# Kernel tuning notes

Hardware: AMD Instinct MI355X
Metric: run time of the kernel (lower is better)

## Reference

```python
import jax, jax.numpy as jnp
import numpy as np


def setup_inputs() -> dict:
    key = jax.random.key(0)
    k1, k2, k3 = jax.random.split(key, 3)
    N, C_in, H, W = 32, 64, 128, 128
    C_out, K = 128, 3
    fan_in = C_in * K * K
    bound = 1.0 / np.sqrt(fan_in)
    x = jax.random.normal(k1, (N, C_in, H, W), dtype=jnp.float32)
    weight = jax.random.uniform(k2, (C_out, C_in, K, K), dtype=jnp.float32, minval=-bound, maxval=bound)
    bias = jax.random.uniform(k3, (C_out,), dtype=jnp.float32, minval=-bound, maxval=bound)
    return {"x": x, "weight": weight, "bias": bias}


def reference(x, weight, bias):
    # conv2d, stride=1, padding=0 (VALID), NCHW / OIHW
    y = jax.lax.conv_general_dilated(
        x, weight,
        window_strides=(1, 1),
        padding='VALID',
        dimension_numbers=('NCHW', 'OIHW', 'NCHW'),
    )
    y = y + bias[None, :, None, None]          # [N, C_out, H_out, W_out]
    y = jnp.min(y, axis=1, keepdims=True)      # channel-wise min -> [N, 1, H_out, W_out]
    return jnp.tanh(jnp.tanh(y))
```

## Files before the change

### kernel.cpp

```cpp
#include <hip/hip_runtime.h>
#include <hip/hip_bf16.h>

typedef __attribute__((ext_vector_type(8))) short short8_t;
typedef __attribute__((ext_vector_type(4))) float floatx4;
typedef unsigned short ushort_t;
typedef unsigned int uint_t;

#define TILE_B 16896

#define RSTR 72
#define TSZ  (132 * RSTR)

__device__ __forceinline__ uint_t rne_u(float f) {
    uint_t u = __float_as_uint(f);
    return u + (0x7fffu + ((u >> 16) & 1u));
}
__device__ __forceinline__ uint_t pk2(float lo, float hi) {
    return __builtin_amdgcn_perm(rne_u(hi), rne_u(lo), 0x07060302u);
}

__global__ void w2_prepass(const float* __restrict__ w, ushort_t* __restrict__ w2) {
    int idx = blockIdx.x * 256 + threadIdx.x;
    int rd  = idx >> 12;
    int rem = idx & 4095;
    int co  = rem >> 5;
    int c32 = rem & 31;
    int khw = rd >> 1, half = rd & 1;
    int ci  = half * 32 + c32;
    w2[idx] = (ushort_t)(rne_u(w[co * 576 + ci * 9 + khw]) >> 16);
}

__global__ __launch_bounds__(256)
void x2_prepass(const float* __restrict__ x, ushort_t* __restrict__ x2) {
    __shared__ __align__(16) float lds[64 * 129];
    const int t = threadIdx.x;
    const int b = blockIdx.x;
    const int n = b >> 7, h = b & 127;
    const float* xp = x + ((size_t)n << 20) + (size_t)h * 128;
#pragma unroll
    for (int r = 0; r < 32; ++r) {
        int flat = r * 256 + t;
        int ci = flat >> 7, wq = flat & 127;
        lds[ci * 129 + wq] = xp[(size_t)ci * 16384 + wq];
    }
    __syncthreads();
    ushort_t* op = x2 + ((size_t)n * 128 + h) * 128 * 64;
#pragma unroll
    for (int r = 0; r < 4; ++r) {
        int id = r * 256 + t;
        int wq = id >> 3, q = id & 7;
        uint_t o[4];
#pragma unroll
        for (int qq = 0; qq < 4; ++qq)
            o[qq] = pk2(lds[(q * 8 + 2 * qq) * 129 + wq],
                        lds[(q * 8 + 2 * qq + 1) * 129 + wq]);
        *reinterpret_cast<uint4*>(op + (size_t)wq * 64 + q * 8) =
            make_uint4(o[0], o[1], o[2], o[3]);
    }
}

__global__ __launch_bounds__(512, 4)
void conv_v3(const ushort_t* __restrict__ x2, const ushort_t* __restrict__ w2,
             const float* __restrict__ bias, float* __restrict__ out)
{
    __shared__ __align__(16) ushort_t T[4 * (TILE_B / 2)];
    __shared__ __align__(16) float red[2][256];

    const int tid  = threadIdx.x;
    const int bid0 = blockIdx.x;
    const int bid  = (bid0 & 7) * 252 + (bid0 >> 3);
    const int n    = bid / 63;
    const int ho0  = (bid - n * 63) * 2;

    const int lane = tid & 63;
    const int wid  = tid >> 6;
    const int wm   = wid >> 1;
    const int wn   = wid & 1;
    const int r16  = lane & 15;
    const int quad = lane >> 4;

    const int voffB = ((lane >> 3) * 128) + (((lane & 7) ^ (lane >> 3)) * 16);
    const ushort_t* xrow = x2 + ((size_t)n * 128 + ho0) * 128 * 64;
#pragma unroll
    for (int s = 0; s < 4; ++s) {
#pragma unroll
        for (int k = 0; k < 2; ++k) {
            const int col0 = (wid * 2 + k) * 8;
            const char* g = (const char*)xrow + (size_t)s * 16384 + col0 * 128 + voffB;
            const ushort_t* l = &T[(s * TILE_B + col0 * 128) / 2];
            __builtin_amdgcn_global_load_lds(
                (const __attribute__((address_space(1))) uint_t*)g,
                (__attribute__((address_space(3))) uint_t*)l, 16, 0, 0);
        }
    }

    {
        const int s = tid >> 7, rem = tid & 127;
        reinterpret_cast<uint_t*>(T)[(s * TILE_B + (128 + (rem >> 5)) * 128) / 4 + (rem & 31)] = 0u;
    }

    floatx4 acc[4][4];
#pragma unroll
    for (int i = 0; i < 4; ++i)
#pragma unroll
        for (int j = 0; j < 4; ++j)
            acc[i][j] = (floatx4){0.f, 0.f, 0.f, 0.f};

    const ushort_t* w2base = w2 + (size_t)(wn * 64 + r16) * 32 + quad * 8;

    const int mc0 = (wm & 1) * 64 + r16;
    const int ms0 = wm >> 1;

    __syncthreads();

#pragma unroll
    for (int rd = 0; rd < 18; ++rd) {
        const int khw  = rd >> 1;
        const int kh   = khw / 3;
        const int kw   = khw - kh * 3;
        const int half = rd & 1;

        short8_t bfr[4];
        {
            const ushort_t* bb = w2base + rd * 4096;
#pragma unroll
            for (int t4 = 0; t4 < 4; ++t4)
                bfr[t4] = *reinterpret_cast<const short8_t*>(bb + t4 * 512);
        }

        short8_t afr[4];
        {
            const int c0 = mc0 + kw;
            const int abase = (ms0 + kh) * TILE_B + c0 * 128
                            + (((half * 4 + quad) ^ (c0 & 7)) * 16);
            const char* ap = (const char*)T + abase;
#pragma unroll
            for (int t4 = 0; t4 < 4; ++t4)
                afr[t4] = *reinterpret_cast<const short8_t*>(ap + t4 * 2048);
        }

#pragma unroll
        for (int tm = 0; tm < 4; ++tm)
#pragma unroll
            for (int tn = 0; tn < 4; ++tn)
                acc[tm][tn] = __builtin_amdgcn_mfma_f32_16x16x32_bf16(
                    afr[tm], bfr[tn], acc[tm][tn], 0, 0, 0);
    }

    float bvv[4];
#pragma unroll
    for (int tn = 0; tn < 4; ++tn)
        bvv[tn] = bias[wn * 64 + tn * 16 + r16];

#pragma unroll
    for (int tm = 0; tm < 4; ++tm) {
#pragma unroll
        for (int r = 0; r < 4; ++r) {
            float v = acc[tm][0][r] + bvv[0];
            v = fminf(v, acc[tm][1][r] + bvv[1]);
            v = fminf(v, acc[tm][2][r] + bvv[2]);
            v = fminf(v, acc[tm][3][r] + bvv[3]);
            v = fminf(v, __shfl_xor(v, 1, 64));
            v = fminf(v, __shfl_xor(v, 2, 64));
            v = fminf(v, __shfl_xor(v, 4, 64));
            v = fminf(v, __shfl_xor(v, 8, 64));
            if (r16 == 0)
                red[wn][wm * 64 + tm * 16 + quad * 4 + r] = v;
        }
    }
    __syncthreads();

    if (tid < 256) {
        const int r  = tid >> 7;
        const int wo = tid & 127;
        if (wo < 126) {
            float v = fminf(red[0][tid], red[1][tid]);
            v = tanhf(tanhf(v));
            out[((size_t)n * 126 + ho0 + r) * 126 + wo] = v;
        }
    }
}

template<bool USE_W2>
__global__ __launch_bounds__(512, 4)
void conv_min_tanh_kernel(const float* __restrict__ x,
                          const float* __restrict__ w,
                          const ushort_t* __restrict__ w2,
                          const float* __restrict__ bias,
                          float* __restrict__ out)
{
    __shared__ __align__(16) ushort_t T[4 * TSZ];
    __shared__ __align__(16) float red[2][256];

    const int tid  = threadIdx.x;
    const int bid0 = blockIdx.x;
    const int bid  = (bid0 & 7) * 252 + (bid0 >> 3);
    const int n    = bid / 63;
    const int ho0  = (bid - n * 63) * 2;

    const int tx = tid & 31;
    const int ty = tid >> 5;

    const int lane = tid & 63;
    const int wid  = tid >> 6;
    const int wm   = wid >> 1;
    const int wn   = wid & 1;
    const int r16  = lane & 15;
    const int quad = lane >> 4;

    const float* xbase = x + ((size_t)n << 20) + (size_t)ho0 * 128;

    auto load_row = [&](floatx4 (&dv)[4], const int s) {
#pragma unroll
        for (int j = 0; j < 4; ++j)
            dv[j] = *reinterpret_cast<const floatx4*>(
                xbase + (size_t)(ty * 4 + j) * 16384 + s * 128 + tx * 4);
    };
    auto conv_row = [&](floatx4 (&dv)[4], const int s) {
#pragma unroll
        for (int i = 0; i < 4; ++i) {
            uint2 u;
            u.x = pk2(dv[0][i], dv[1][i]);
            u.y = pk2(dv[2][i], dv[3][i]);
            const int c   = tx * 4 + i;
            const int swz = (ty >> 1) ^ ((c >> 3) & 7);
            *reinterpret_cast<uint2*>(&T[s * TSZ + c * RSTR + swz * 8 + (ty & 1) * 4]) = u;
        }
    };

    floatx4 dva[4], dvb[4];
    load_row(dva, 0);
    load_row(dvb, 1);

    for (int idx = tid; idx < 576; idx += 512) {
        int s = idx / 144, o = idx - s * 144;
        reinterpret_cast<uint_t*>(T)[s * (TSZ / 2) + (128 * RSTR) / 2 + o] = 0u;
    }

    conv_row(dva, 0);
    load_row(dva, 2);
    conv_row(dvb, 1);
    load_row(dvb, 3);
    conv_row(dva, 2);
    conv_row(dvb, 3);

    floatx4 acc[4][4];
#pragma unroll
    for (int i = 0; i < 4; ++i)
#pragma unroll
        for (int j = 0; j < 4; ++j)
            acc[i][j] = (floatx4){0.f, 0.f, 0.f, 0.f};

    const ushort_t* w2base = w2 + (size_t)(wn * 64 + r16) * 32 + quad * 8;
    const float*    wbase  = w + (size_t)(wn * 64 + r16) * 576;

    __syncthreads();

#pragma unroll
    for (int rd = 0; rd < 18; ++rd) {
        const int khw  = rd >> 1;
        const int kh   = khw / 3;
        const int kw   = khw - kh * 3;
        const int half = rd & 1;

        short8_t bfr[4];
        if (USE_W2) {
            const ushort_t* bb = w2base + rd * 4096;
#pragma unroll
            for (int t4 = 0; t4 < 4; ++t4)
                bfr[t4] = *reinterpret_cast<const short8_t*>(bb + t4 * 512);
        } else {
#pragma unroll
            for (int t4 = 0; t4 < 4; ++t4) {
                const float* wp = wbase + (size_t)t4 * (16 * 576)
                                + (size_t)(half * 32 + quad * 8) * 9 + khw;
                short8_t b;
#pragma unroll
                for (int q = 0; q < 4; ++q) {
                    uint_t u = pk2(wp[(2 * q) * 9], wp[(2 * q + 1) * 9]);
                    b[2 * q]     = (short)(u & 0xffffu);
                    b[2 * q + 1] = (short)(u >> 16);
                }
                bfr[t4] = b;
            }
        }

        short8_t afr[4];
#pragma unroll
        for (int t4 = 0; t4 < 4; ++t4) {
            const int m  = wm * 64 + t4 * 16 + r16;
            const int s  = (m >> 7) + kh;
            const int c  = (m & 127) + kw;
            const int sw = (half * 4 + quad) ^ ((c >> 3) & 7);
            afr[t4] = *reinterpret_cast<const short8_t*>(&T[s * TSZ + c * RSTR + sw * 8]);
        }
#pragma unroll
        for (int tm = 0; tm < 4; ++tm)
#pragma unroll
            for (int tn = 0; tn < 4; ++tn)
                acc[tm][tn] = __builtin_amdgcn_mfma_f32_16x16x32_bf16(
                    afr[tm], bfr[tn], acc[tm][tn], 0, 0, 0);
    }

    float bvv[4];
#pragma unroll
    for (int tn = 0; tn < 4; ++tn)
        bvv[tn] = bias[wn * 64 + tn * 16 + r16];

#pragma unroll
    for (int tm = 0; tm < 4; ++tm) {
#pragma unroll
        for (int r = 0; r < 4; ++r) {
            float v = acc[tm][0][r] + bvv[0];
            v = fminf(v, acc[tm][1][r] + bvv[1]);
            v = fminf(v, acc[tm][2][r] + bvv[2]);
            v = fminf(v, acc[tm][3][r] + bvv[3]);
            v = fminf(v, __shfl_xor(v, 1, 64));
            v = fminf(v, __shfl_xor(v, 2, 64));
            v = fminf(v, __shfl_xor(v, 4, 64));
            v = fminf(v, __shfl_xor(v, 8, 64));
            if (r16 == 0)
                red[wn][wm * 64 + tm * 16 + quad * 4 + r] = v;
        }
    }
    __syncthreads();

    if (tid < 256) {
        const int r  = tid >> 7;
        const int wo = tid & 127;
        if (wo < 126) {
            float v = fminf(red[0][tid], red[1][tid]);
            v = tanhf(tanhf(v));
            out[((size_t)n * 126 + ho0 + r) * 126 + wo] = v;
        }
    }
}

extern "C" void kernel_launch(void* const* d_in, const int* in_sizes, int n_in,
                              void* d_out, int out_size, void* d_ws, size_t ws_size,
                              hipStream_t stream) {
    const float* x    = (const float*)d_in[0];
    const float* w    = (const float*)d_in[1];
    const float* bias = (const float*)d_in[2];
    float* out = (float*)d_out;

    const size_t X2B = (size_t)32 * 128 * 128 * 64 * 2;
    const size_t W2B = (size_t)73728 * 2;

    if (ws_size >= X2B + W2B) {
        ushort_t* x2 = (ushort_t*)d_ws;
        ushort_t* w2 = (ushort_t*)((char*)d_ws + X2B);
        x2_prepass<<<dim3(4096), dim3(256), 0, stream>>>(x, x2);
        w2_prepass<<<dim3(288), dim3(256), 0, stream>>>(w, w2);
        conv_v3<<<dim3(2016), dim3(512), 0, stream>>>(x2, w2, bias, out);
    } else if (ws_size >= W2B) {
        ushort_t* w2 = (ushort_t*)d_ws;
        w2_prepass<<<dim3(288), dim3(256), 0, stream>>>(w, w2);
        conv_min_tanh_kernel<true><<<dim3(2016), dim3(512), 0, stream>>>(x, w, (ushort_t*)d_ws, bias, out);
    } else {
        conv_min_tanh_kernel<false><<<dim3(2016), dim3(512), 0, stream>>>(x, w, nullptr, bias, out);
    }
}
```

Baseline: 284.5 us.

## Process six output rows per block with rolling LDS ring and fused prepass

Each conv block now computes three consecutive output row-pairs, keeping a 4-slot ring of bf16 input rows in LDS. It refills the next two rows via global_load_lds partway through each pass, so each input row is loaded about once instead of roughly twice. Weight fragments are software-prefetched one step ahead, and the x and w bf16 prepasses are merged into one launch. The grid shrinks from 2016 to 672 blocks, which reduces parallelism and tail balance, and the mid-loop barrier may stall waves.

```diff
diff --git a/kernel.cpp b/kernel.cpp
--- a/kernel.cpp
+++ b/kernel.cpp
@@ -17,6 +17,208 @@
 }
 __device__ __forceinline__ uint_t pk2(float lo, float hi) {
     return __builtin_amdgcn_perm(rne_u(hi), rne_u(lo), 0x07060302u);
+}
+
+__global__ __launch_bounds__(256)
+void prepass_fused(const float* __restrict__ x, const float* __restrict__ w,
+                   ushort_t* __restrict__ x2, ushort_t* __restrict__ w2)
+{
+    __shared__ __align__(16) float lds[64 * 129];
+    const int t = threadIdx.x;
+    const int b = blockIdx.x;
+    if (b >= 4096) {
+        int idx = (b - 4096) * 256 + t;
+        int rd  = idx >> 12;
+        int rem = idx & 4095;
+        int co  = rem >> 5;
+        int c32 = rem & 31;
+        int khw = rd >> 1, half = rd & 1;
+        int ci  = half * 32 + c32;
+        w2[idx] = (ushort_t)(rne_u(w[co * 576 + ci * 9 + khw]) >> 16);
+        return;
+    }
+    const int n = b >> 7, h = b & 127;
+    const float* xp = x + ((size_t)n << 20) + (size_t)h * 128;
+#pragma unroll
+    for (int r = 0; r < 16; ++r) {
+        int flat = r * 256 + t;
+        int ci = flat >> 6, wh = flat & 63;
+        float2 v = *reinterpret_cast<const float2*>(xp + (size_t)ci * 16384 + wh * 2);
+        lds[ci * 129 + wh * 2]     = v.x;
+        lds[ci * 129 + wh * 2 + 1] = v.y;
+    }
+    __syncthreads();
+    ushort_t* op = x2 + ((size_t)n * 128 + h) * 8192;
+#pragma unroll
+    for (int r = 0; r < 4; ++r) {
+        int id = r * 256 + t;
+        int wq = id >> 3, q = id & 7;
+        uint_t o[4];
+#pragma unroll
+        for (int qq = 0; qq < 4; ++qq)
+            o[qq] = pk2(lds[(q * 8 + 2 * qq) * 129 + wq],
+                        lds[(q * 8 + 2 * qq + 1) * 129 + wq]);
+        *reinterpret_cast<uint4*>(op + (size_t)wq * 64 + q * 8) =
+            make_uint4(o[0], o[1], o[2], o[3]);
+    }
+}
+
+__global__ __launch_bounds__(512, 4)
+void conv_v4(const ushort_t* __restrict__ x2, const ushort_t* __restrict__ w2,
+             const float* __restrict__ bias, float* __restrict__ out)
+{
+    __shared__ __align__(16) ushort_t T[4 * (TILE_B / 2)];
+    __shared__ __align__(16) float red[2][256];
+
+    const int tid  = threadIdx.x;
+    const int bid0 = blockIdx.x;
+    const int bid  = (bid0 & 7) * 84 + (bid0 >> 3);
+    const int n    = bid / 21;
+    const int pg   = bid - n * 21;
+    const int ho0  = pg * 6;
+
+    const int lane = tid & 63;
+    const int wid  = tid >> 6;
+    const int wm   = wid >> 1;
+    const int wn   = wid & 1;
+    const int r16  = lane & 15;
+    const int quad = lane >> 4;
+    const int ms0  = wm >> 1;
+    const int mc0  = (wm & 1) * 64 + r16;
+
+    const int voffB = ((lane >> 3) * 128) + (((lane & 7) ^ (lane >> 3)) * 16);
+    const ushort_t* xrow = x2 + ((size_t)n * 128 + ho0) * 8192;
+
+#pragma unroll
+    for (int s = 0; s < 4; ++s)
+#pragma unroll
+        for (int k = 0; k < 2; ++k) {
+            const int col0 = (wid * 2 + k) * 8;
+            const char* g = (const char*)xrow + (size_t)s * 16384 + col0 * 128 + voffB;
+            const ushort_t* l = &T[(s * TILE_B + col0 * 128) / 2];
+            __builtin_amdgcn_global_load_lds(
+                (const __attribute__((address_space(1))) uint_t*)g,
+                (__attribute__((address_space(3))) uint_t*)l, 16, 0, 0);
+        }
+
+    {
+        const int s = tid >> 7, rem = tid & 127;
+        reinterpret_cast<uint_t*>(T)[(s * TILE_B + (128 + (rem >> 5)) * 128) / 4 + (rem & 31)] = 0u;
+    }
+
+    floatx4 acc[4][4];
+#pragma unroll
+    for (int i = 0; i < 4; ++i)
+#pragma unroll
+        for (int j = 0; j < 4; ++j)
+            acc[i][j] = (floatx4){0.f, 0.f, 0.f, 0.f};
+
+    const ushort_t* w2base = w2 + (size_t)(wn * 64 + r16) * 32 + quad * 8;
+
+    short8_t bcur[4], bnxt[4];
+#pragma unroll
+    for (int t4 = 0; t4 < 4; ++t4)
+        bcur[t4] = *reinterpret_cast<const short8_t*>(w2base + t4 * 512);
+
+    __syncthreads();
+
+#pragma unroll 1
+    for (int j = 0; j < 3; ++j) {
+#pragma unroll
+        for (int rd = 0; rd < 18; ++rd) {
+            {
+                const int nxt = (rd + 1) % 18;
+                const ushort_t* bb = w2base + nxt * 4096;
+#pragma unroll
+                for (int t4 = 0; t4 < 4; ++t4)
+                    bnxt[t4] = *reinterpret_cast<const short8_t*>(bb + t4 * 512);
+            }
+            const int khw  = rd >> 1;
+            const int kh   = khw / 3;
+            const int kw   = khw - kh * 3;
+            const int half = rd & 1;
+
+            short8_t afr[4];
+            {
+                const int sl = (2 * j + kh + ms0) & 3;
+                const int c0 = mc0 + kw;
+                const int abase = sl * TILE_B + c0 * 128
+                                + (((half * 4 + quad) ^ (c0 & 7)) * 16);
+                const char* ap = (const char*)T + abase;
+#pragma unroll
+                for (int t4 = 0; t4 < 4; ++t4)
+                    afr[t4] = *reinterpret_cast<const short8_t*>(ap + t4 * 2048);
+            }
+#pragma unroll
+            for (int tm = 0; tm < 4; ++tm)
+#pragma unroll
+                for (int tn = 0; tn < 4; ++tn)
+                    acc[tm][tn] = __builtin_amdgcn_mfma_f32_16x16x32_bf16(
+                        afr[tm], bcur[tn], acc[tm][tn], 0, 0, 0);
+#pragma unroll
+            for (int t4 = 0; t4 < 4; ++t4)
+                bcur[t4] = bnxt[t4];
+
+            if (rd == 11) {
+                __syncthreads();
+                if (j < 2) {
+                    const int lr = 2 * j + 4;
+#pragma unroll
+                    for (int rr = 0; rr < 2; ++rr)
+#pragma unroll
+                        for (int k = 0; k < 2; ++k) {
+                            const int col0 = (wid * 2 + k) * 8;
+                            const char* g = (const char*)xrow
+                                + (size_t)(lr + rr) * 16384 + col0 * 128 + voffB;
+                            const ushort_t* l =
+                                &T[(((lr + rr) & 3) * TILE_B + col0 * 128) / 2];
+                            __builtin_amdgcn_global_load_lds(
+                                (const __attribute__((address_space(1))) uint_t*)g,
+                                (__attribute__((address_space(3))) uint_t*)l, 16, 0, 0);
+                        }
+                }
+            }
+        }
+
+        float bvv[4];
+#pragma unroll
+        for (int tn = 0; tn < 4; ++tn)
+            bvv[tn] = bias[wn * 64 + tn * 16 + r16];
+
+#pragma unroll
+        for (int tm = 0; tm < 4; ++tm) {
+#pragma unroll
+            for (int r = 0; r < 4; ++r) {
+                float v = acc[tm][0][r] + bvv[0];
+                v = fminf(v, acc[tm][1][r] + bvv[1]);
+                v = fminf(v, acc[tm][2][r] + bvv[2]);
+                v = fminf(v, acc[tm][3][r] + bvv[3]);
+                v = fminf(v, __shfl_xor(v, 1, 64));
+                v = fminf(v, __shfl_xor(v, 2, 64));
+                v = fminf(v, __shfl_xor(v, 4, 64));
+                v = fminf(v, __shfl_xor(v, 8, 64));
+                if (r16 == 0)
+                    red[wn][wm * 64 + tm * 16 + quad * 4 + r] = v;
+            }
+        }
+        __syncthreads();
+
+        if (tid < 256) {
+            const int r  = tid >> 7;
+            const int wo = tid & 127;
+            if (wo < 126) {
+                float v = fminf(red[0][tid], red[1][tid]);
+                v = tanhf(tanhf(v));
+                out[((size_t)n * 126 + ho0 + 2 * j + r) * 126 + wo] = v;
+            }
+        }
+
+#pragma unroll
+        for (int i = 0; i < 4; ++i)
+#pragma unroll
+            for (int k = 0; k < 4; ++k)
+                acc[i][k] = (floatx4){0.f, 0.f, 0.f, 0.f};
+    }
 }
 
 __global__ void w2_prepass(const float* __restrict__ w, ushort_t* __restrict__ w2) {
@@ -30,40 +232,15 @@
     w2[idx] = (ushort_t)(rne_u(w[co * 576 + ci * 9 + khw]) >> 16);
 }
 
-__global__ __launch_bounds__(256)
-void x2_prepass(const float* __restrict__ x, ushort_t* __restrict__ x2) {
-    __shared__ __align__(16) float lds[64 * 129];
-    const int t = threadIdx.x;
-    const int b = blockIdx.x;
-    const int n = b >> 7, h = b & 127;
-    const float* xp = x + ((size_t)n << 20) + (size_t)h * 128;
-#pragma unroll
-    for (int r = 0; r < 32; ++r) {
-        int flat = r * 256 + t;
-        int ci = flat >> 7, wq = flat & 127;
-        lds[ci * 129 + wq] = xp[(size_t)ci * 16384 + wq];
-    }
-    __syncthreads();
-    ushort_t* op = x2 + ((size_t)n * 128 + h) * 128 * 64;
-#pragma unroll
-    for (int r = 0; r < 4; ++r) {
-        int id = r * 256 + t;
-        int wq = id >> 3, q = id & 7;
-        uint_t o[4];
-#pragma unroll
-        for (int qq = 0; qq < 4; ++qq)
-            o[qq] = pk2(lds[(q * 8 + 2 * qq) * 129 + wq],
-                        lds[(q * 8 + 2 * qq + 1) * 129 + wq]);
-        *reinterpret_cast<uint4*>(op + (size_t)wq * 64 + q * 8) =
-            make_uint4(o[0], o[1], o[2], o[3]);
-    }
-}
-
+template<bool USE_W2>
 __global__ __launch_bounds__(512, 4)
-void conv_v3(const ushort_t* __restrict__ x2, const ushort_t* __restrict__ w2,
-             const float* __restrict__ bias, float* __restrict__ out)
+void conv_min_tanh_kernel(const float* __restrict__ x,
+                          const float* __restrict__ w,
+                          const ushort_t* __restrict__ w2,
+                          const float* __restrict__ bias,
+                          float* __restrict__ out)
 {
-    __shared__ __align__(16) ushort_t T[4 * (TILE_B / 2)];
+    __shared__ __align__(16) ushort_t T[4 * TSZ];
     __shared__ __align__(16) float red[2][256];
 
     const int tid  = threadIdx.x;
@@ -71,6 +248,9 @@
     const int bid  = (bid0 & 7) * 252 + (bid0 >> 3);
     const int n    = bid / 63;
     const int ho0  = (bid - n * 63) * 2;
+
+    const int tx = tid & 31;
+    const int ty = tid >> 5;
 
     const int lane = tid & 63;
     const int wid  = tid >> 6;
@@ -79,25 +259,41 @@
     const int r16  = lane & 15;
     const int quad = lane >> 4;
 
-    const int voffB = ((lane >> 3) * 128) + (((lane & 7) ^ (lane >> 3)) * 16);
-    const ushort_t* xrow = x2 + ((size_t)n * 128 + ho0) * 128 * 64;
-#pragma unroll
-    for (int s = 0; s < 4; ++s) {
-#pragma unroll
-        for (int k = 0; k < 2; ++k) {
-            const int col0 = (wid * 2 + k) * 8;
-            const char* g = (const char*)xrow + (size_t)s * 16384 + col0 * 128 + voffB;
-            const ushort_t* l = &T[(s * TILE_B + col0 * 128) / 2];
-            __builtin_amdgcn_global_load_lds(
-                (const __attribute__((address_space(1))) uint_t*)g,
-                (__attribute__((address_space(3))) uint_t*)l, 16, 0, 0);
-        }
-    }
-
-    {
-        const int s = tid >> 7, rem = tid & 127;
-        reinterpret_cast<uint_t*>(T)[(s * TILE_B + (128 + (rem >> 5)) * 128) / 4 + (rem & 31)] = 0u;
-    }
+    const float* xbase = x + ((size_t)n << 20) + (size_t)ho0 * 128;
+
+    auto load_row = [&](floatx4 (&dv)[4], const int s) {
+#pragma unroll
+        for (int j = 0; j < 4; ++j)
+            dv[j] = *reinterpret_cast<const floatx4*>(
+                xbase + (size_t)(ty * 4 + j) * 16384 + s * 128 + tx * 4);
+    };
+    auto conv_row = [&](floatx4 (&dv)[4], const int s) {
+#pragma unroll
+        for (int i = 0; i < 4; ++i) {
+            uint2 u;
+            u.x = pk2(dv[0][i], dv[1][i]);
+            u.y = pk2(dv[2][i], dv[3][i]);
+            const int c   = tx * 4 + i;
+            const int swz = (ty >> 1) ^ ((c >> 3) & 7);
+            *reinterpret_cast<uint2*>(&T[s * TSZ + c * RSTR + swz * 8 + (ty & 1) * 4]) = u;
+        }
+    };
+
+    floatx4 dva[4], dvb[4];
+    load_row(dva, 0);
+    load_row(dvb, 1);
+
+    for (int idx = tid; idx < 576; idx += 512) {
+        int s = idx / 144, o = idx - s * 144;
+        reinterpret_cast<uint_t*>(T)[s * (TSZ / 2) + (128 * RSTR) / 2 + o] = 0u;
+    }
+
+    conv_row(dva, 0);
+    load_row(dva, 2);
+    conv_row(dvb, 1);
+    load_row(dvb, 3);
+    conv_row(dva, 2);
+    conv_row(dvb, 3);
 
     floatx4 acc[4][4];
 #pragma unroll
@@ -107,9 +303,7 @@
             acc[i][j] = (floatx4){0.f, 0.f, 0.f, 0.f};
 
     const ushort_t* w2base = w2 + (size_t)(wn * 64 + r16) * 32 + quad * 8;
-
-    const int mc0 = (wm & 1) * 64 + r16;
-    const int ms0 = wm >> 1;
+    const float*    wbase  = w + (size_t)(wn * 64 + r16) * 576;
 
     __syncthreads();
 
@@ -121,24 +315,36 @@
         const int half = rd & 1;
 
         short8_t bfr[4];
-        {
+        if (USE_W2) {
             const ushort_t* bb = w2base + rd * 4096;
 #pragma unroll
             for (int t4 = 0; t4 < 4; ++t4)
                 bfr[t4] = *reinterpret_cast<const short8_t*>(bb + t4 * 512);
+        } else {
+#pragma unroll
+            for (int t4 = 0; t4 < 4; ++t4) {
+                const float* wp = wbase + (size_t)t4 * (16 * 576)
+                                + (size_t)(half * 32 + quad * 8) * 9 + khw;
+                short8_t b;
+#pragma unroll
+                for (int q = 0; q < 4; ++q) {
+                    uint_t u = pk2(wp[(2 * q) * 9], wp[(2 * q + 1) * 9]);
+                    b[2 * q]     = (short)(u & 0xffffu);
+                    b[2 * q + 1] = (short)(u >> 16);
+                }
+                bfr[t4] = b;
+            }
         }
 
         short8_t afr[4];
-        {
-            const int c0 = mc0 + kw;
-            const int abase = (ms0 + kh) * TILE_B + c0 * 128
-                            + (((half * 4 + quad) ^ (c0 & 7)) * 16);
-            const char* ap = (const char*)T + abase;
-#pragma unroll
-            for (int t4 = 0; t4 < 4; ++t4)
-                afr[t4] = *reinterpret_cast<const short8_t*>(ap + t4 * 2048);
-        }
-
+#pragma unroll
+        for (int t4 = 0; t4 < 4; ++t4) {
+            const int m  = wm * 64 + t4 * 16 + r16;
+            const int s  = (m >> 7) + kh;
+            const int c  = (m & 127) + kw;
+            const int sw = (half * 4 + quad) ^ ((c >> 3) & 7);
+            afr[t4] = *reinterpret_cast<const short8_t*>(&T[s * TSZ + c * RSTR + sw * 8]);
+        }
 #pragma unroll
         for (int tm = 0; tm < 4; ++tm)
 #pragma unroll
@@ -181,161 +387,6 @@
     }
 }
 
-template<bool USE_W2>
-__global__ __launch_bounds__(512, 4)
-void conv_min_tanh_kernel(const float* __restrict__ x,
-                          const float* __restrict__ w,
-                          const ushort_t* __restrict__ w2,
-                          const float* __restrict__ bias,
-                          float* __restrict__ out)
-{
-    __shared__ __align__(16) ushort_t T[4 * TSZ];
-    __shared__ __align__(16) float red[2][256];
-
-    const int tid  = threadIdx.x;
-    const int bid0 = blockIdx.x;
-    const int bid  = (bid0 & 7) * 252 + (bid0 >> 3);
-    const int n    = bid / 63;
-    const int ho0  = (bid - n * 63) * 2;
-
-    const int tx = tid & 31;
-    const int ty = tid >> 5;
-
-    const int lane = tid & 63;
-    const int wid  = tid >> 6;
-    const int wm   = wid >> 1;
-    const int wn   = wid & 1;
-    const int r16  = lane & 15;
-    const int quad = lane >> 4;
-
-    const float* xbase = x + ((size_t)n << 20) + (size_t)ho0 * 128;
-
-    auto load_row = [&](floatx4 (&dv)[4], const int s) {
-#pragma unroll
-        for (int j = 0; j < 4; ++j)
-            dv[j] = *reinterpret_cast<const floatx4*>(
-                xbase + (size_t)(ty * 4 + j) * 16384 + s * 128 + tx * 4);
-    };
-    auto conv_row = [&](floatx4 (&dv)[4], const int s) {
-#pragma unroll
-        for (int i = 0; i < 4; ++i) {
-            uint2 u;
-            u.x = pk2(dv[0][i], dv[1][i]);
-            u.y = pk2(dv[2][i], dv[3][i]);
-            const int c   = tx * 4 + i;
-            const int swz = (ty >> 1) ^ ((c >> 3) & 7);
-            *reinterpret_cast<uint2*>(&T[s * TSZ + c * RSTR + swz * 8 + (ty & 1) * 4]) = u;
-        }
-    };
-
-    floatx4 dva[4], dvb[4];
-    load_row(dva, 0);
-    load_row(dvb, 1);
-
-    for (int idx = tid; idx < 576; idx += 512) {
-        int s = idx / 144, o = idx - s * 144;
-        reinterpret_cast<uint_t*>(T)[s * (TSZ / 2) + (128 * RSTR) / 2 + o] = 0u;
-    }
-
-    conv_row(dva, 0);
-    load_row(dva, 2);
-    conv_row(dvb, 1);
-    load_row(dvb, 3);
-    conv_row(dva, 2);
-    conv_row(dvb, 3);
-
-    floatx4 acc[4][4];
-#pragma unroll
-    for (int i = 0; i < 4; ++i)
-#pragma unroll
-        for (int j = 0; j < 4; ++j)
-            acc[i][j] = (floatx4){0.f, 0.f, 0.f, 0.f};
-
-    const ushort_t* w2base = w2 + (size_t)(wn * 64 + r16) * 32 + quad * 8;
-    const float*    wbase  = w + (size_t)(wn * 64 + r16) * 576;
-
-    __syncthreads();
-
-#pragma unroll
-    for (int rd = 0; rd < 18; ++rd) {
-        const int khw  = rd >> 1;
-        const int kh   = khw / 3;
-        const int kw   = khw - kh * 3;
-        const int half = rd & 1;
-
-        short8_t bfr[4];
-        if (USE_W2) {
-            const ushort_t* bb = w2base + rd * 4096;
-#pragma unroll
-            for (int t4 = 0; t4 < 4; ++t4)
-                bfr[t4] = *reinterpret_cast<const short8_t*>(bb + t4 * 512);
-        } else {
-#pragma unroll
-            for (int t4 = 0; t4 < 4; ++t4) {
-                const float* wp = wbase + (size_t)t4 * (16 * 576)
-                                + (size_t)(half * 32 + quad * 8) * 9 + khw;
-                short8_t b;
-#pragma unroll
-                for (int q = 0; q < 4; ++q) {
-                    uint_t u = pk2(wp[(2 * q) * 9], wp[(2 * q + 1) * 9]);
-                    b[2 * q]     = (short)(u & 0xffffu);
-                    b[2 * q + 1] = (short)(u >> 16);
-                }
-                bfr[t4] = b;
-            }
-        }
-
-        short8_t afr[4];
-#pragma unroll
-        for (int t4 = 0; t4 < 4; ++t4) {
-            const int m  = wm * 64 + t4 * 16 + r16;
-            const int s  = (m >> 7) + kh;
-            const int c  = (m & 127) + kw;
-            const int sw = (half * 4 + quad) ^ ((c >> 3) & 7);
-            afr[t4] = *reinterpret_cast<const short8_t*>(&T[s * TSZ + c * RSTR + sw * 8]);
-        }
-#pragma unroll
-        for (int tm = 0; tm < 4; ++tm)
-#pragma unroll
-            for (int tn = 0; tn < 4; ++tn)
-                acc[tm][tn] = __builtin_amdgcn_mfma_f32_16x16x32_bf16(
-                    afr[tm], bfr[tn], acc[tm][tn], 0, 0, 0);
-    }
-
-    float bvv[4];
-#pragma unroll
-    for (int tn = 0; tn < 4; ++tn)
-        bvv[tn] = bias[wn * 64 + tn * 16 + r16];
-
-#pragma unroll
-    for (int tm = 0; tm < 4; ++tm) {
-#pragma unroll
-        for (int r = 0; r < 4; ++r) {
-            float v = acc[tm][0][r] + bvv[0];
-            v = fminf(v, acc[tm][1][r] + bvv[1]);
-            v = fminf(v, acc[tm][2][r] + bvv[2]);
-            v = fminf(v, acc[tm][3][r] + bvv[3]);
-            v = fminf(v, __shfl_xor(v, 1, 64));
-            v = fminf(v, __shfl_xor(v, 2, 64));
-            v = fminf(v, __shfl_xor(v, 4, 64));
-            v = fminf(v, __shfl_xor(v, 8, 64));
-            if (r16 == 0)
-                red[wn][wm * 64 + tm * 16 + quad * 4 + r] = v;
-        }
-    }
-    __syncthreads();
-
-    if (tid < 256) {
-        const int r  = tid >> 7;
-        const int wo = tid & 127;
-        if (wo < 126) {
-            float v = fminf(red[0][tid], red[1][tid]);
-            v = tanhf(tanhf(v));
-            out[((size_t)n * 126 + ho0 + r) * 126 + wo] = v;
-        }
-    }
-}
-
 extern "C" void kernel_launch(void* const* d_in, const int* in_sizes, int n_in,
                               void* d_out, int out_size, void* d_ws, size_t ws_size,
                               hipStream_t stream) {
@@ -350,13 +401,12 @@
     if (ws_size >= X2B + W2B) {
         ushort_t* x2 = (ushort_t*)d_ws;
         ushort_t* w2 = (ushort_t*)((char*)d_ws + X2B);
-        x2_prepass<<<dim3(4096), dim3(256), 0, stream>>>(x, x2);
-        w2_prepass<<<dim3(288), dim3(256), 0, stream>>>(w, w2);
-        conv_v3<<<dim3(2016), dim3(512), 0, stream>>>(x2, w2, bias, out);
+        prepass_fused<<<dim3(4096 + 288), dim3(256), 0, stream>>>(x, w, x2, w2);
+        conv_v4<<<dim3(672), dim3(512), 0, stream>>>(x2, w2, bias, out);
     } else if (ws_size >= W2B) {
         ushort_t* w2 = (ushort_t*)d_ws;
         w2_prepass<<<dim3(288), dim3(256), 0, stream>>>(w, w2);
-        conv_min_tanh_kernel<true><<<dim3(2016), dim3(512), 0, stream>>>(x, w, (ushort_t*)d_ws, bias, out);
+        conv_min_tanh_kernel<true><<<dim3(2016), dim3(512), 0, stream>>>(x, w, w2, bias, out);
     } else {
         conv_min_tanh_kernel<false><<<dim3(2016), dim3(512), 0, stream>>>(x, w, nullptr, bias, out);
     }
```

After: 555.6 us. 1.95x slower.

## Fuse input/weight prepasses and shrink conv tile to one output row per block

Applied to the files above, without the earlier changes.

The x and weight bf16 conversion prepasses are merged into a single launch, with float2 loads in the x transpose, removing one kernel launch. The conv kernel now computes one output row per block instead of two. It loads 3 input rows into LDS instead of 4, halving the accumulator registers and LDS per block and raising the occupancy hint from 4 to 6 blocks. This trades more input-row reloads across blocks (3 rows per output row instead of 2) for higher occupancy, twice as many blocks and less register pressure.

```diff
diff --git a/kernel.cpp b/kernel.cpp
--- a/kernel.cpp
+++ b/kernel.cpp
@@ -17,6 +17,166 @@
 }
 __device__ __forceinline__ uint_t pk2(float lo, float hi) {
     return __builtin_amdgcn_perm(rne_u(hi), rne_u(lo), 0x07060302u);
+}
+
+__global__ __launch_bounds__(256)
+void prepass_fused(const float* __restrict__ x, const float* __restrict__ w,
+                   ushort_t* __restrict__ x2, ushort_t* __restrict__ w2)
+{
+    __shared__ __align__(16) float lds[64 * 129];
+    const int t = threadIdx.x;
+    const int b = blockIdx.x;
+    if (b >= 4096) {
+        int idx = (b - 4096) * 256 + t;
+        int rd  = idx >> 12;
+        int rem = idx & 4095;
+        int co  = rem >> 5;
+        int c32 = rem & 31;
+        int khw = rd >> 1, half = rd & 1;
+        int ci  = half * 32 + c32;
+        w2[idx] = (ushort_t)(rne_u(w[co * 576 + ci * 9 + khw]) >> 16);
+        return;
+    }
+    const int n = b >> 7, h = b & 127;
+    const float* xp = x + ((size_t)n << 20) + (size_t)h * 128;
+#pragma unroll
+    for (int r = 0; r < 16; ++r) {
+        int flat = r * 256 + t;
+        int ci = flat >> 6, wh = flat & 63;
+        float2 v = *reinterpret_cast<const float2*>(xp + (size_t)ci * 16384 + wh * 2);
+        lds[ci * 129 + wh * 2]     = v.x;
+        lds[ci * 129 + wh * 2 + 1] = v.y;
+    }
+    __syncthreads();
+    ushort_t* op = x2 + ((size_t)n * 128 + h) * 8192;
+#pragma unroll
+    for (int r = 0; r < 4; ++r) {
+        int id = r * 256 + t;
+        int wq = id >> 3, q = id & 7;
+        uint_t o[4];
+#pragma unroll
+        for (int qq = 0; qq < 4; ++qq)
+            o[qq] = pk2(lds[(q * 8 + 2 * qq) * 129 + wq],
+                        lds[(q * 8 + 2 * qq + 1) * 129 + wq]);
+        *reinterpret_cast<uint4*>(op + (size_t)wq * 64 + q * 8) =
+            make_uint4(o[0], o[1], o[2], o[3]);
+    }
+}
+
+__global__ __launch_bounds__(512, 6)
+void conv_v5(const ushort_t* __restrict__ x2, const ushort_t* __restrict__ w2,
+             const float* __restrict__ bias, float* __restrict__ out)
+{
+    __shared__ __align__(16) ushort_t T[3 * (TILE_B / 2)];
+    __shared__ __align__(16) float red[2][128];
+
+    const int tid  = threadIdx.x;
+    const int bid0 = blockIdx.x;
+    const int bid  = (bid0 & 7) * 504 + (bid0 >> 3);
+    const int n    = bid / 126;
+    const int ho   = bid - n * 126;
+
+    const int lane = tid & 63;
+    const int wid  = tid >> 6;
+    const int wm   = wid >> 1;
+    const int wn   = wid & 1;
+    const int r16  = lane & 15;
+    const int quad = lane >> 4;
+    const int mc0  = wm * 32 + r16;
+
+    const int voffB = ((lane >> 3) * 128) + (((lane & 7) ^ (lane >> 3)) * 16);
+    const ushort_t* xrow = x2 + ((size_t)n * 128 + ho) * 8192;
+
+#pragma unroll
+    for (int s = 0; s < 3; ++s)
+#pragma unroll
+        for (int k = 0; k < 2; ++k) {
+            const int col0 = (wid * 2 + k) * 8;
+            const char* g = (const char*)xrow + (size_t)s * 16384 + col0 * 128 + voffB;
+            const ushort_t* l = &T[(s * TILE_B + col0 * 128) / 2];
+            __builtin_amdgcn_global_load_lds(
+                (const __attribute__((address_space(1))) uint_t*)g,
+                (__attribute__((address_space(3))) uint_t*)l, 16, 0, 0);
+        }
+
+    if (tid < 384) {
+        const int s = tid / 128, rem = tid & 127;
+        reinterpret_cast<uint_t*>(T)[(s * TILE_B + (128 + (rem >> 5)) * 128) / 4 + (rem & 31)] = 0u;
+    }
+
+    floatx4 acc[2][4];
+#pragma unroll
+    for (int i = 0; i < 2; ++i)
+#pragma unroll
+        for (int j = 0; j < 4; ++j)
+            acc[i][j] = (floatx4){0.f, 0.f, 0.f, 0.f};
+
+    const ushort_t* w2base = w2 + (size_t)(wn * 64 + r16) * 32 + quad * 8;
+
+    __syncthreads();
+
+#pragma unroll
+    for (int rd = 0; rd < 18; ++rd) {
+        const int khw  = rd >> 1;
+        const int kh   = khw / 3;
+        const int kw   = khw - kh * 3;
+        const int half = rd & 1;
+
+        short8_t bfr[4];
+        {
+            const ushort_t* bb = w2base + rd * 4096;
+#pragma unroll
+            for (int t4 = 0; t4 < 4; ++t4)
+                bfr[t4] = *reinterpret_cast<const short8_t*>(bb + t4 * 512);
+        }
+
+        short8_t afr[2];
+        {
+            const int c0 = mc0 + kw;
+            const int abase = kh * TILE_B + c0 * 128
+                            + (((half * 4 + quad) ^ (c0 & 7)) * 16);
+            const char* ap = (const char*)T + abase;
+#pragma unroll
+            for (int t4 = 0; t4 < 2; ++t4)
+                afr[t4] = *reinterpret_cast<const short8_t*>(ap + t4 * 2048);
+        }
+
+#pragma unroll
+        for (int tm = 0; tm < 2; ++tm)
+#pragma unroll
+            for (int tn = 0; tn < 4; ++tn)
+                acc[tm][tn] = __builtin_amdgcn_mfma_f32_16x16x32_bf16(
+                    afr[tm], bfr[tn], acc[tm][tn], 0, 0, 0);
+    }
+
+    float bvv[4];
+#pragma unroll
+    for (int tn = 0; tn < 4; ++tn)
+        bvv[tn] = bias[wn * 64 + tn * 16 + r16];
+
+#pragma unroll
+    for (int tm = 0; tm < 2; ++tm) {
+#pragma unroll
+        for (int r = 0; r < 4; ++r) {
+            float v = acc[tm][0][r] + bvv[0];
+            v = fminf(v, acc[tm][1][r] + bvv[1]);
+            v = fminf(v, acc[tm][2][r] + bvv[2]);
+            v = fminf(v, acc[tm][3][r] + bvv[3]);
+            v = fminf(v, __shfl_xor(v, 1, 64));
+            v = fminf(v, __shfl_xor(v, 2, 64));
+            v = fminf(v, __shfl_xor(v, 4, 64));
+            v = fminf(v, __shfl_xor(v, 8, 64));
+            if (r16 == 0)
+                red[wn][wm * 32 + tm * 16 + quad * 4 + r] = v;
+        }
+    }
+    __syncthreads();
+
+    if (tid < 126) {
+        float v = fminf(red[0][tid], red[1][tid]);
+        v = tanhf(tanhf(v));
+        out[((size_t)n * 126 + ho) * 126 + tid] = v;
+    }
 }
 
 __global__ void w2_prepass(const float* __restrict__ w, ushort_t* __restrict__ w2) {
@@ -30,40 +190,15 @@
     w2[idx] = (ushort_t)(rne_u(w[co * 576 + ci * 9 + khw]) >> 16);
 }
 
-__global__ __launch_bounds__(256)
-void x2_prepass(const float* __restrict__ x, ushort_t* __restrict__ x2) {
-    __shared__ __align__(16) float lds[64 * 129];
-    const int t = threadIdx.x;
-    const int b = blockIdx.x;
-    const int n = b >> 7, h = b & 127;
-    const float* xp = x + ((size_t)n << 20) + (size_t)h * 128;
-#pragma unroll
-    for (int r = 0; r < 32; ++r) {
-        int flat = r * 256 + t;
-        int ci = flat >> 7, wq = flat & 127;
-        lds[ci * 129 + wq] = xp[(size_t)ci * 16384 + wq];
-    }
-    __syncthreads();
-    ushort_t* op = x2 + ((size_t)n * 128 + h) * 128 * 64;
-#pragma unroll
-    for (int r = 0; r < 4; ++r) {
-        int id = r * 256 + t;
-        int wq = id >> 3, q = id & 7;
-        uint_t o[4];
-#pragma unroll
-        for (int qq = 0; qq < 4; ++qq)
-            o[qq] = pk2(lds[(q * 8 + 2 * qq) * 129 + wq],
-                        lds[(q * 8 + 2 * qq + 1) * 129 + wq]);
-        *reinterpret_cast<uint4*>(op + (size_t)wq * 64 + q * 8) =
-            make_uint4(o[0], o[1], o[2], o[3]);
-    }
-}
-
+template<bool USE_W2>
 __global__ __launch_bounds__(512, 4)
-void conv_v3(const ushort_t* __restrict__ x2, const ushort_t* __restrict__ w2,
-             const float* __restrict__ bias, float* __restrict__ out)
+void conv_min_tanh_kernel(const float* __restrict__ x,
+                          const float* __restrict__ w,
+                          const ushort_t* __restrict__ w2,
+                          const float* __restrict__ bias,
+                          float* __restrict__ out)
 {
-    __shared__ __align__(16) ushort_t T[4 * (TILE_B / 2)];
+    __shared__ __align__(16) ushort_t T[4 * TSZ];
     __shared__ __align__(16) float red[2][256];
 
     const int tid  = threadIdx.x;
@@ -71,6 +206,9 @@
     const int bid  = (bid0 & 7) * 252 + (bid0 >> 3);
     const int n    = bid / 63;
     const int ho0  = (bid - n * 63) * 2;
+
+    const int tx = tid & 31;
+    const int ty = tid >> 5;
 
     const int lane = tid & 63;
     const int wid  = tid >> 6;
@@ -79,25 +217,41 @@
     const int r16  = lane & 15;
     const int quad = lane >> 4;
 
-    const int voffB = ((lane >> 3) * 128) + (((lane & 7) ^ (lane >> 3)) * 16);
-    const ushort_t* xrow = x2 + ((size_t)n * 128 + ho0) * 128 * 64;
-#pragma unroll
-    for (int s = 0; s < 4; ++s) {
-#pragma unroll
-        for (int k = 0; k < 2; ++k) {
-            const int col0 = (wid * 2 + k) * 8;
-            const char* g = (const char*)xrow + (size_t)s * 16384 + col0 * 128 + voffB;
-            const ushort_t* l = &T[(s * TILE_B + col0 * 128) / 2];
-            __builtin_amdgcn_global_load_lds(
-                (const __attribute__((address_space(1))) uint_t*)g,
-                (__attribute__((address_space(3))) uint_t*)l, 16, 0, 0);
-        }
-    }
-
-    {
-        const int s = tid >> 7, rem = tid & 127;
-        reinterpret_cast<uint_t*>(T)[(s * TILE_B + (128 + (rem >> 5)) * 128) / 4 + (rem & 31)] = 0u;
-    }
+    const float* xbase = x + ((size_t)n << 20) + (size_t)ho0 * 128;
+
+    auto load_row = [&](floatx4 (&dv)[4], const int s) {
+#pragma unroll
+        for (int j = 0; j < 4; ++j)
+            dv[j] = *reinterpret_cast<const floatx4*>(
+                xbase + (size_t)(ty * 4 + j) * 16384 + s * 128 + tx * 4);
+    };
+    auto conv_row = [&](floatx4 (&dv)[4], const int s) {
+#pragma unroll
+        for (int i = 0; i < 4; ++i) {
+            uint2 u;
+            u.x = pk2(dv[0][i], dv[1][i]);
+            u.y = pk2(dv[2][i], dv[3][i]);
+            const int c   = tx * 4 + i;
+            const int swz = (ty >> 1) ^ ((c >> 3) & 7);
+            *reinterpret_cast<uint2*>(&T[s * TSZ + c * RSTR + swz * 8 + (ty & 1) * 4]) = u;
+        }
+    };
+
+    floatx4 dva[4], dvb[4];
+    load_row(dva, 0);
+    load_row(dvb, 1);
+
+    for (int idx = tid; idx < 576; idx += 512) {
+        int s = idx / 144, o = idx - s * 144;
+        reinterpret_cast<uint_t*>(T)[s * (TSZ / 2) + (128 * RSTR) / 2 + o] = 0u;
+    }
+
+    conv_row(dva, 0);
+    load_row(dva, 2);
+    conv_row(dvb, 1);
+    load_row(dvb, 3);
+    conv_row(dva, 2);
+    conv_row(dvb, 3);
 
     floatx4 acc[4][4];
 #pragma unroll
@@ -107,9 +261,7 @@
             acc[i][j] = (floatx4){0.f, 0.f, 0.f, 0.f};
 
     const ushort_t* w2base = w2 + (size_t)(wn * 64 + r16) * 32 + quad * 8;
-
-    const int mc0 = (wm & 1) * 64 + r16;
-    const int ms0 = wm >> 1;
+    const float*    wbase  = w + (size_t)(wn * 64 + r16) * 576;
 
     __syncthreads();
 
@@ -121,24 +273,36 @@
         const int half = rd & 1;
 
         short8_t bfr[4];
-        {
+        if (USE_W2) {
             const ushort_t* bb = w2base + rd * 4096;
 #pragma unroll
             for (int t4 = 0; t4 < 4; ++t4)
                 bfr[t4] = *reinterpret_cast<const short8_t*>(bb + t4 * 512);
+        } else {
+#pragma unroll
+            for (int t4 = 0; t4 < 4; ++t4) {
+                const float* wp = wbase + (size_t)t4 * (16 * 576)
+                                + (size_t)(half * 32 + quad * 8) * 9 + khw;
+                short8_t b;
+#pragma unroll
+                for (int q = 0; q < 4; ++q) {
+                    uint_t u = pk2(wp[(2 * q) * 9], wp[(2 * q + 1) * 9]);
+                    b[2 * q]     = (short)(u & 0xffffu);
+                    b[2 * q + 1] = (short)(u >> 16);
+                }
+                bfr[t4] = b;
+            }
         }
 
         short8_t afr[4];
-        {
-            const int c0 = mc0 + kw;
-            const int abase = (ms0 + kh) * TILE_B + c0 * 128
-                            + (((half * 4 + quad) ^ (c0 & 7)) * 16);
-            const char* ap = (const char*)T + abase;
-#pragma unroll
-            for (int t4 = 0; t4 < 4; ++t4)
-                afr[t4] = *reinterpret_cast<const short8_t*>(ap + t4 * 2048);
-        }
-
+#pragma unroll
+        for (int t4 = 0; t4 < 4; ++t4) {
+            const int m  = wm * 64 + t4 * 16 + r16;
+            const int s  = (m >> 7) + kh;
+            const int c  = (m & 127) + kw;
+            const int sw = (half * 4 + quad) ^ ((c >> 3) & 7);
+            afr[t4] = *reinterpret_cast<const short8_t*>(&T[s * TSZ + c * RSTR + sw * 8]);
+        }
 #pragma unroll
         for (int tm = 0; tm < 4; ++tm)
 #pragma unroll
@@ -181,161 +345,6 @@
     }
 }
 
-template<bool USE_W2>
-__global__ __launch_bounds__(512, 4)
-void conv_min_tanh_kernel(const float* __restrict__ x,
-                          const float* __restrict__ w,
-                          const ushort_t* __restrict__ w2,
-                          const float* __restrict__ bias,
-                          float* __restrict__ out)
-{
-    __shared__ __align__(16) ushort_t T[4 * TSZ];
-    __shared__ __align__(16) float red[2][256];
-
-    const int tid  = threadIdx.x;
-    const int bid0 = blockIdx.x;
-    const int bid  = (bid0 & 7) * 252 + (bid0 >> 3);
-    const int n    = bid / 63;
-    const int ho0  = (bid - n * 63) * 2;
-
-    const int tx = tid & 31;
-    const int ty = tid >> 5;
-
-    const int lane = tid & 63;
-    const int wid  = tid >> 6;
-    const int wm   = wid >> 1;
-    const int wn   = wid & 1;
-    const int r16  = lane & 15;
-    const int quad = lane >> 4;
-
-    const float* xbase = x + ((size_t)n << 20) + (size_t)ho0 * 128;
-
-    auto load_row = [&](floatx4 (&dv)[4], const int s) {
-#pragma unroll
-        for (int j = 0; j < 4; ++j)
-            dv[j] = *reinterpret_cast<const floatx4*>(
-                xbase + (size_t)(ty * 4 + j) * 16384 + s * 128 + tx * 4);
-    };
-    auto conv_row = [&](floatx4 (&dv)[4], const int s) {
-#pragma unroll
-        for (int i = 0; i < 4; ++i) {
-            uint2 u;
-            u.x = pk2(dv[0][i], dv[1][i]);
-            u.y = pk2(dv[2][i], dv[3][i]);
-            const int c   = tx * 4 + i;
-            const int swz = (ty >> 1) ^ ((c >> 3) & 7);
-            *reinterpret_cast<uint2*>(&T[s * TSZ + c * RSTR + swz * 8 + (ty & 1) * 4]) = u;
-        }
-    };
-
-    floatx4 dva[4], dvb[4];
-    load_row(dva, 0);
-    load_row(dvb, 1);
-
-    for (int idx = tid; idx < 576; idx += 512) {
-        int s = idx / 144, o = idx - s * 144;
-        reinterpret_cast<uint_t*>(T)[s * (TSZ / 2) + (128 * RSTR) / 2 + o] = 0u;
-    }
-
-    conv_row(dva, 0);
-    load_row(dva, 2);
-    conv_row(dvb, 1);
-    load_row(dvb, 3);
-    conv_row(dva, 2);
-    conv_row(dvb, 3);
-
-    floatx4 acc[4][4];
-#pragma unroll
-    for (int i = 0; i < 4; ++i)
-#pragma unroll
-        for (int j = 0; j < 4; ++j)
-            acc[i][j] = (floatx4){0.f, 0.f, 0.f, 0.f};
-
-    const ushort_t* w2base = w2 + (size_t)(wn * 64 + r16) * 32 + quad * 8;
-    const float*    wbase  = w + (size_t)(wn * 64 + r16) * 576;
-
-    __syncthreads();
-
-#pragma unroll
-    for (int rd = 0; rd < 18; ++rd) {
-        const int khw  = rd >> 1;
-        const int kh   = khw / 3;
-        const int kw   = khw - kh * 3;
-        const int half = rd & 1;
-
-        short8_t bfr[4];
-        if (USE_W2) {
-            const ushort_t* bb = w2base + rd * 4096;
-#pragma unroll
-            for (int t4 = 0; t4 < 4; ++t4)
-                bfr[t4] = *reinterpret_cast<const short8_t*>(bb + t4 * 512);
-        } else {
-#pragma unroll
-            for (int t4 = 0; t4 < 4; ++t4) {
-                const float* wp = wbase + (size_t)t4 * (16 * 576)
-                                + (size_t)(half * 32 + quad * 8) * 9 + khw;
-                short8_t b;
-#pragma unroll
-                for (int q = 0; q < 4; ++q) {
-                    uint_t u = pk2(wp[(2 * q) * 9], wp[(2 * q + 1) * 9]);
-                    b[2 * q]     = (short)(u & 0xffffu);
-                    b[2 * q + 1] = (short)(u >> 16);
-                }
-                bfr[t4] = b;
-            }
-        }
-
-        short8_t afr[4];
-#pragma unroll
-        for (int t4 = 0; t4 < 4; ++t4) {
-            const int m  = wm * 64 + t4 * 16 + r16;
-            const int s  = (m >> 7) + kh;
-            const int c  = (m & 127) + kw;
-            const int sw = (half * 4 + quad) ^ ((c >> 3) & 7);
-            afr[t4] = *reinterpret_cast<const short8_t*>(&T[s * TSZ + c * RSTR + sw * 8]);
-        }
-#pragma unroll
-        for (int tm = 0; tm < 4; ++tm)
-#pragma unroll
-            for (int tn = 0; tn < 4; ++tn)
-                acc[tm][tn] = __builtin_amdgcn_mfma_f32_16x16x32_bf16(
-                    afr[tm], bfr[tn], acc[tm][tn], 0, 0, 0);
-    }
-
-    float bvv[4];
-#pragma unroll
-    for (int tn = 0; tn < 4; ++tn)
-        bvv[tn] = bias[wn * 64 + tn * 16 + r16];
-
-#pragma unroll
-    for (int tm = 0; tm < 4; ++tm) {
-#pragma unroll
-        for (int r = 0; r < 4; ++r) {
-            float v = acc[tm][0][r] + bvv[0];
-            v = fminf(v, acc[tm][1][r] + bvv[1]);
-            v = fminf(v, acc[tm][2][r] + bvv[2]);
-            v = fminf(v, acc[tm][3][r] + bvv[3]);
-            v = fminf(v, __shfl_xor(v, 1, 64));
-            v = fminf(v, __shfl_xor(v, 2, 64));
-            v = fminf(v, __shfl_xor(v, 4, 64));
-            v = fminf(v, __shfl_xor(v, 8, 64));
-            if (r16 == 0)
-                red[wn][wm * 64 + tm * 16 + quad * 4 + r] = v;
-        }
-    }
-    __syncthreads();
-
-    if (tid < 256) {
-        const int r  = tid >> 7;
-        const int wo = tid & 127;
-        if (wo < 126) {
-            float v = fminf(red[0][tid], red[1][tid]);
-            v = tanhf(tanhf(v));
-            out[((size_t)n * 126 + ho0 + r) * 126 + wo] = v;
-        }
-    }
-}
-
 extern "C" void kernel_launch(void* const* d_in, const int* in_sizes, int n_in,
                               void* d_out, int out_size, void* d_ws, size_t ws_size,
                               hipStream_t stream) {
@@ -350,13 +359,12 @@
     if (ws_size >= X2B + W2B) {
         ushort_t* x2 = (ushort_t*)d_ws;
         ushort_t* w2 = (ushort_t*)((char*)d_ws + X2B);
-        x2_prepass<<<dim3(4096), dim3(256), 0, stream>>>(x, x2);
-        w2_prepass<<<dim3(288), dim3(256), 0, stream>>>(w, w2);
-        conv_v3<<<dim3(2016), dim3(512), 0, stream>>>(x2, w2, bias, out);
+        prepass_fused<<<dim3(4096 + 288), dim3(256), 0, stream>>>(x, w, x2, w2);
+        conv_v5<<<dim3(4032), dim3(512), 0, stream>>>(x2, w2, bias, out);
     } else if (ws_size >= W2B) {
         ushort_t* w2 = (ushort_t*)d_ws;
         w2_prepass<<<dim3(288), dim3(256), 0, stream>>>(w, w2);
-        conv_min_tanh_kernel<true><<<dim3(2016), dim3(512), 0, stream>>>(x, w, (ushort_t*)d_ws, bias, out);
+        conv_min_tanh_kernel<true><<<dim3(2016), dim3(512), 0, stream>>>(x, w, w2, bias, out);
     } else {
         conv_min_tanh_kernel<false><<<dim3(2016), dim3(512), 0, stream>>>(x, w, nullptr, bias, out);
     }
```

Result: slower. 334.8 us (+17.7%).

## Fuse weight and input prepasses into one launch, prefetch B fragments, widen loads

Applied to the files above, without the earlier changes.

Merges the weight-conversion and input-transposition prepasses into a single kernel launch, with the extra blocks handling the weights, so one launch and its gap go away. The input prepass now reads float2 per thread, halving the load loop count. In the conv kernel, the weight fragments for the next reduction step are double-buffered in registers so global/L2 latency overlaps the MFMAs, at the cost of extra VGPRs under the 4-wave occupancy bound.

```diff
diff --git a/kernel.cpp b/kernel.cpp
--- a/kernel.cpp
+++ b/kernel.cpp
@@ -19,32 +19,36 @@
     return __builtin_amdgcn_perm(rne_u(hi), rne_u(lo), 0x07060302u);
 }
 
-__global__ void w2_prepass(const float* __restrict__ w, ushort_t* __restrict__ w2) {
-    int idx = blockIdx.x * 256 + threadIdx.x;
-    int rd  = idx >> 12;
-    int rem = idx & 4095;
-    int co  = rem >> 5;
-    int c32 = rem & 31;
-    int khw = rd >> 1, half = rd & 1;
-    int ci  = half * 32 + c32;
-    w2[idx] = (ushort_t)(rne_u(w[co * 576 + ci * 9 + khw]) >> 16);
-}
-
 __global__ __launch_bounds__(256)
-void x2_prepass(const float* __restrict__ x, ushort_t* __restrict__ x2) {
+void prepass_fused(const float* __restrict__ x, const float* __restrict__ w,
+                   ushort_t* __restrict__ x2, ushort_t* __restrict__ w2)
+{
     __shared__ __align__(16) float lds[64 * 129];
     const int t = threadIdx.x;
     const int b = blockIdx.x;
+    if (b >= 4096) {
+        int idx = (b - 4096) * 256 + t;
+        int rd  = idx >> 12;
+        int rem = idx & 4095;
+        int co  = rem >> 5;
+        int c32 = rem & 31;
+        int khw = rd >> 1, half = rd & 1;
+        int ci  = half * 32 + c32;
+        w2[idx] = (ushort_t)(rne_u(w[co * 576 + ci * 9 + khw]) >> 16);
+        return;
+    }
     const int n = b >> 7, h = b & 127;
     const float* xp = x + ((size_t)n << 20) + (size_t)h * 128;
 #pragma unroll
-    for (int r = 0; r < 32; ++r) {
+    for (int r = 0; r < 16; ++r) {
         int flat = r * 256 + t;
-        int ci = flat >> 7, wq = flat & 127;
-        lds[ci * 129 + wq] = xp[(size_t)ci * 16384 + wq];
-    }
-    __syncthreads();
-    ushort_t* op = x2 + ((size_t)n * 128 + h) * 128 * 64;
+        int ci = flat >> 6, wh = flat & 63;
+        float2 v = *reinterpret_cast<const float2*>(xp + (size_t)ci * 16384 + wh * 2);
+        lds[ci * 129 + wh * 2]     = v.x;
+        lds[ci * 129 + wh * 2 + 1] = v.y;
+    }
+    __syncthreads();
+    ushort_t* op = x2 + ((size_t)n * 128 + h) * 8192;
 #pragma unroll
     for (int r = 0; r < 4; ++r) {
         int id = r * 256 + t;
@@ -60,7 +64,7 @@
 }
 
 __global__ __launch_bounds__(512, 4)
-void conv_v3(const ushort_t* __restrict__ x2, const ushort_t* __restrict__ w2,
+void conv_v7(const ushort_t* __restrict__ x2, const ushort_t* __restrict__ w2,
              const float* __restrict__ bias, float* __restrict__ out)
 {
     __shared__ __align__(16) ushort_t T[4 * (TILE_B / 2)];
@@ -80,9 +84,9 @@
     const int quad = lane >> 4;
 
     const int voffB = ((lane >> 3) * 128) + (((lane & 7) ^ (lane >> 3)) * 16);
-    const ushort_t* xrow = x2 + ((size_t)n * 128 + ho0) * 128 * 64;
-#pragma unroll
-    for (int s = 0; s < 4; ++s) {
+    const ushort_t* xrow = x2 + ((size_t)n * 128 + ho0) * 8192;
+#pragma unroll
+    for (int s = 0; s < 4; ++s)
 #pragma unroll
         for (int k = 0; k < 2; ++k) {
             const int col0 = (wid * 2 + k) * 8;
@@ -92,7 +96,6 @@
                 (const __attribute__((address_space(1))) uint_t*)g,
                 (__attribute__((address_space(3))) uint_t*)l, 16, 0, 0);
         }
-    }
 
     {
         const int s = tid >> 7, rem = tid & 127;
@@ -111,22 +114,26 @@
     const int mc0 = (wm & 1) * 64 + r16;
     const int ms0 = wm >> 1;
 
+    short8_t bcur[4], bnxt[4];
+#pragma unroll
+    for (int t4 = 0; t4 < 4; ++t4)
+        bcur[t4] = *reinterpret_cast<const short8_t*>(w2base + t4 * 512);
+
     __syncthreads();
 
 #pragma unroll
     for (int rd = 0; rd < 18; ++rd) {
+        if (rd < 17) {
+            const ushort_t* bb = w2base + (rd + 1) * 4096;
+#pragma unroll
+            for (int t4 = 0; t4 < 4; ++t4)
+                bnxt[t4] = *reinterpret_cast<const short8_t*>(bb + t4 * 512);
+        }
+
         const int khw  = rd >> 1;
         const int kh   = khw / 3;
         const int kw   = khw - kh * 3;
         const int half = rd & 1;
-
-        short8_t bfr[4];
-        {
-            const ushort_t* bb = w2base + rd * 4096;
-#pragma unroll
-            for (int t4 = 0; t4 < 4; ++t4)
-                bfr[t4] = *reinterpret_cast<const short8_t*>(bb + t4 * 512);
-        }
 
         short8_t afr[4];
         {
@@ -144,7 +151,11 @@
 #pragma unroll
             for (int tn = 0; tn < 4; ++tn)
                 acc[tm][tn] = __builtin_amdgcn_mfma_f32_16x16x32_bf16(
-                    afr[tm], bfr[tn], acc[tm][tn], 0, 0, 0);
+                    afr[tm], bcur[tn], acc[tm][tn], 0, 0, 0);
+
+#pragma unroll
+        for (int t4 = 0; t4 < 4; ++t4)
+            bcur[t4] = bnxt[t4];
     }
 
     float bvv[4];
@@ -181,6 +192,17 @@
     }
 }
 
+__global__ void w2_prepass(const float* __restrict__ w, ushort_t* __restrict__ w2) {
+    int idx = blockIdx.x * 256 + threadIdx.x;
+    int rd  = idx >> 12;
+    int rem = idx & 4095;
+    int co  = rem >> 5;
+    int c32 = rem & 31;
+    int khw = rd >> 1, half = rd & 1;
+    int ci  = half * 32 + c32;
+    w2[idx] = (ushort_t)(rne_u(w[co * 576 + ci * 9 + khw]) >> 16);
+}
+
 template<bool USE_W2>
 __global__ __launch_bounds__(512, 4)
 void conv_min_tanh_kernel(const float* __restrict__ x,
@@ -350,13 +372,12 @@
     if (ws_size >= X2B + W2B) {
         ushort_t* x2 = (ushort_t*)d_ws;
         ushort_t* w2 = (ushort_t*)((char*)d_ws + X2B);
-        x2_prepass<<<dim3(4096), dim3(256), 0, stream>>>(x, x2);
-        w2_prepass<<<dim3(288), dim3(256), 0, stream>>>(w, w2);
-        conv_v3<<<dim3(2016), dim3(512), 0, stream>>>(x2, w2, bias, out);
+        prepass_fused<<<dim3(4096 + 288), dim3(256), 0, stream>>>(x, w, x2, w2);
+        conv_v7<<<dim3(2016), dim3(512), 0, stream>>>(x2, w2, bias, out);
     } else if (ws_size >= W2B) {
         ushort_t* w2 = (ushort_t*)d_ws;
         w2_prepass<<<dim3(288), dim3(256), 0, stream>>>(w, w2);
-        conv_min_tanh_kernel<true><<<dim3(2016), dim3(512), 0, stream>>>(x, w, (ushort_t*)d_ws, bias, out);
+        conv_min_tanh_kernel<true><<<dim3(2016), dim3(512), 0, stream>>>(x, w, w2, bias, out);
     } else {
         conv_min_tanh_kernel<false><<<dim3(2016), dim3(512), 0, stream>>>(x, w, nullptr, bias, out);
     }
```

After: 276.3 us. -2.9%, faster.
